# Optimization experiments

Measured on AMD Instinct MI355X. Metric: run time of the kernel, lower is better.

The kernel has to match this reference:

```python
import jax, jax.numpy as jnp
import numpy as np
from jax import lax

N_NODES, IN_FEATS = 10000, 768
B, P, MAXLEN = 2048, 16384, 50
V, D, NF, HID = 50000, 300, 100, 64


def setup_inputs() -> dict:
    key = jax.random.key(0)
    ks = jax.random.split(key, 17)
    emb = jax.random.normal(ks[4], (V, D), jnp.float32) * 0.1
    emb = emb.at[0].set(0.0)  # padding_idx=0
    return {
        'x': jax.random.normal(ks[0], (N_NODES, IN_FEATS), jnp.float32),
        'rootindex': jax.random.randint(ks[1], (B,), 0, N_NODES),
        'hist_tokens': jax.random.randint(ks[2], (P, MAXLEN), 0, V),
        'segment_ids': jnp.sort(jax.random.randint(ks[3], (P,), 0, B)),
        'emb_table': emb,
        'conv_w3': jax.random.normal(ks[5], (NF, D, 3), jnp.float32) * 0.02,
        'conv_b3': jax.random.normal(ks[6], (NF,), jnp.float32) * 0.02,
        'conv_w4': jax.random.normal(ks[7], (NF, D, 4), jnp.float32) * 0.02,
        'conv_b4': jax.random.normal(ks[8], (NF,), jnp.float32) * 0.02,
        'conv_w5': jax.random.normal(ks[9], (NF, D, 5), jnp.float32) * 0.02,
        'conv_b5': jax.random.normal(ks[10], (NF,), jnp.float32) * 0.02,
        'hist_w': jax.random.normal(ks[11], (HID, 3 * NF), jnp.float32) * 0.05,
        'hist_b': jax.random.normal(ks[12], (HID,), jnp.float32) * 0.02,
        'fc_w1': jax.random.normal(ks[13], (2 * HID, IN_FEATS), jnp.float32) * 0.03,
        'fc_b1': jax.random.normal(ks[14], (2 * HID,), jnp.float32) * 0.02,
        'fc_w2': jax.random.normal(ks[15], (HID, 2 * HID), jnp.float32) * 0.08,
        'fc_b2': jax.random.normal(ks[16], (HID,), jnp.float32) * 0.02,
    }


def reference(x, rootindex, hist_tokens, segment_ids, emb_table,
              conv_w3, conv_b3, conv_w4, conv_b4, conv_w5, conv_b5,
              hist_w, hist_b, fc_w1, fc_b1, fc_w2, fc_b2):
    nseg = rootindex.shape[0]  # B users
    # --- hist_aggregation: ragged per-user embedding lookup + mean over posts ---
    emb = emb_table[hist_tokens]                                   # [P, L, D]
    sums = jax.ops.segment_sum(emb, segment_ids, num_segments=nseg)  # [B, L, D]
    counts = jax.ops.segment_sum(jnp.ones((segment_ids.shape[0],), emb.dtype),
                                 segment_ids, num_segments=nseg)
    hist = sums / jnp.maximum(counts, 1.0)[:, None, None]          # [B, L, D]
    # --- records_aggregation: TextCNN over [B, D, L] ---
    xr = jnp.transpose(hist, (0, 2, 1))                            # [B, D, L]
    feats = []
    for w, b in ((conv_w3, conv_b3), (conv_w4, conv_b4), (conv_w5, conv_b5)):
        c = lax.conv_general_dilated(xr, w, (1,), 'VALID',
                                     dimension_numbers=('NCH', 'OIH', 'NCH'))
        c = jax.nn.relu(c + b[None, :, None])                      # [B, NF, L-K+1]
        feats.append(jnp.max(c, axis=-1))                          # global max pool
    f = jnp.concatenate(feats, axis=1)                             # [B, 3*NF]
    rec = f @ hist_w.T + hist_b                                    # [B, 64]
    # --- fc_out on root node features (dropout = eval no-op) ---
    h = jax.nn.relu(x[rootindex] @ fc_w1.T + fc_b1)                # [B, 128]
    out_fc = h @ fc_w2.T + fc_b2                                   # [B, 64]
    return rec + out_fc
```

## Files before the change

### kernel.cpp

```cpp
#include <hip/hip_runtime.h>

#define NB    2048
#define NP    16384
#define LL    50
#define DD    300
#define DP    320
#define TP    52
#define NTOT  300
#define NPADF 320
#define INFEAT 768
#define HID2  128
#define UPB   4
#define FCM   16

typedef short v8s __attribute__((ext_vector_type(8)));
typedef float v4f __attribute__((ext_vector_type(4)));
typedef float v2f __attribute__((ext_vector_type(2)));
typedef unsigned short v4u __attribute__((ext_vector_type(4)));

__device__ __forceinline__ unsigned short f2bf(float f) {
    union { float f; unsigned u; } v; v.f = f;
    return (unsigned short)((v.u + 0x7FFF + ((v.u >> 16) & 1)) >> 16);
}
__device__ __forceinline__ float bf2f(unsigned short u) {
    union { unsigned u; float f; } v; v.u = ((unsigned)u) << 16; return v.f;
}
__device__ __forceinline__ int lower_bound_i(const int* __restrict__ a, int n, int v) {
    int lo = 0, hi = n;
    while (lo < hi) { int mid = (lo + hi) >> 1; if (a[mid] < v) lo = mid + 1; else hi = mid; }
    return lo;
}

__device__ __forceinline__ void async_copy16(const void* g, void* l) {
    __builtin_amdgcn_global_load_lds(
        (const __attribute__((address_space(1))) unsigned int*)g,
        (__attribute__((address_space(3))) unsigned int*)l, 16, 0, 0);
}

__global__ void emb_cvt8(const float* __restrict__ in, unsigned* __restrict__ out, int n4) {
    for (int i = blockIdx.x * blockDim.x + threadIdx.x; i < n4; i += gridDim.x * blockDim.x) {
        float4 v = ((const float4*)in)[i];
        int o = 0;
        o = __builtin_amdgcn_cvt_pk_fp8_f32(v.x, v.y, o, false);
        o = __builtin_amdgcn_cvt_pk_fp8_f32(v.z, v.w, o, true);
        out[i] = (unsigned)o;
    }
}

__global__ void prep_w(const float* __restrict__ w3, const float* __restrict__ w4,
                       const float* __restrict__ w5,
                       const float* __restrict__ b3, const float* __restrict__ b4,
                       const float* __restrict__ b5,
                       unsigned short* __restrict__ W5f, float* __restrict__ bias_all,
                       const float* __restrict__ fw1, unsigned short* __restrict__ w1b) {
    int idx = blockIdx.x * blockDim.x + threadIdx.x;
    if (idx < HID2 * INFEAT / 4) {
        float4 v = ((const float4*)fw1)[idx];
        ushort4 o; o.x = f2bf(v.x); o.y = f2bf(v.y); o.z = f2bf(v.z); o.w = f2bf(v.w);
        ((ushort4*)w1b)[idx] = o;
    }
    if (idx < NPADF) {
        float bv = 0.f;
        if (idx < 100) bv = b3[idx];
        else if (idx < 200) bv = b4[idx - 100];
        else if (idx < 300) bv = b5[idx - 200];
        bias_all[idx] = bv;
    }
    if (idx >= 10 * 5 * 20 * 512) return;
    int j    = idx & 7;
    int lane = (idx >> 3) & 63;
    int rest = idx >> 9;
    int nt = rest % 20;
    int s  = (rest / 20) % 5;
    int kt = rest / 100;
    int col = lane & 15, quad = lane >> 4;
    int nf = nt * 16 + col;
    int d  = kt * 32 + quad * 8 + j;
    float v = 0.f;
    if (nf < NTOT && d < DD) {
        int cls = nf / 100, f = nf % 100, K = cls + 3;
        if (s < K) {
            const float* w = (cls == 0) ? w3 : (cls == 1) ? w4 : w5;
            v = w[(f * DD + d) * K + s];
        }
    }
    W5f[idx] = f2bf(v);
}

#define PCHUNK 32
__global__ __launch_bounds__(512, 1) void gather_kernel(
    const int* __restrict__ hist_tokens, const int* __restrict__ seg,
    const unsigned char* __restrict__ emb8, unsigned short* __restrict__ histb)
{
    __shared__ int tokoff[PCHUNK * LL];
    const int b = blockIdx.x, tid = threadIdx.x;
    const int lo = lower_bound_i(seg, NP, b);
    const int hi = lower_bound_i(seg, NP, b + 1);
    const float inv = 1.0f / fmaxf((float)(hi - lo), 1.0f);

    int toff[8], doff[8];
    #pragma unroll
    for (int j = 0; j < 8; ++j) {
        int idx = tid + 512 * j;
        if (idx < 3750) { toff[j] = idx / 75; doff[j] = (idx % 75) * 4; }
        else            { toff[j] = 0;        doff[j] = 0; }
    }
    const bool has8 = (tid < 166);

    float4 acc[8];
    #pragma unroll
    for (int j = 0; j < 8; ++j) acc[j] = make_float4(0.f, 0.f, 0.f, 0.f);

    for (int p0 = lo; p0 < hi; p0 += PCHUNK) {
        const int pc = min(PCHUNK, hi - p0);
        __syncthreads();
        for (int j = tid; j < pc * LL; j += 512)
            tokoff[j] = hist_tokens[p0 * LL + j] * DD;
        __syncthreads();
        int pp = 0;
        for (; pp + 1 < pc; pp += 2) {
            const int* trA = tokoff + pp * LL;
            const int* trB = trA + LL;
            unsigned va[8], vb[8];
            #pragma unroll
            for (int j = 0; j < 7; ++j)
                va[j] = *(const unsigned*)(emb8 + trA[toff[j]] + doff[j]);
            if (has8) va[7] = *(const unsigned*)(emb8 + trA[toff[7]] + doff[7]);
            #pragma unroll
            for (int j = 0; j < 7; ++j)
                vb[j] = *(const unsigned*)(emb8 + trB[toff[j]] + doff[j]);
            if (has8) vb[7] = *(const unsigned*)(emb8 + trB[toff[7]] + doff[7]);
            #pragma unroll
            for (int j = 0; j < 8; ++j) {
                if (j < 7 || has8) {
                    v2f la = __builtin_amdgcn_cvt_pk_f32_fp8(va[j], false);
                    v2f ha = __builtin_amdgcn_cvt_pk_f32_fp8(va[j], true);
                    v2f lb = __builtin_amdgcn_cvt_pk_f32_fp8(vb[j], false);
                    v2f hb2 = __builtin_amdgcn_cvt_pk_f32_fp8(vb[j], true);
                    acc[j].x += la[0] + lb[0];
                    acc[j].y += la[1] + lb[1];
                    acc[j].z += ha[0] + hb2[0];
                    acc[j].w += ha[1] + hb2[1];
                }
            }
        }
        if (pp < pc) {
            const int* tr = tokoff + pp * LL;
            unsigned v[8];
            #pragma unroll
            for (int j = 0; j < 7; ++j)
                v[j] = *(const unsigned*)(emb8 + tr[toff[j]] + doff[j]);
            if (has8) v[7] = *(const unsigned*)(emb8 + tr[toff[7]] + doff[7]);
            #pragma unroll
            for (int j = 0; j < 8; ++j) {
                if (j < 7 || has8) {
                    v2f lv = __builtin_amdgcn_cvt_pk_f32_fp8(v[j], false);
                    v2f hv = __builtin_amdgcn_cvt_pk_f32_fp8(v[j], true);
                    acc[j].x += lv[0]; acc[j].y += lv[1];
                    acc[j].z += hv[0]; acc[j].w += hv[1];
                }
            }
        }
    }

    unsigned short* hb = histb + (size_t)b * TP * DP;
    #pragma unroll
    for (int j = 0; j < 8; ++j) {
        if (j < 7 || has8) {
            v4u o;
            o[0] = f2bf(acc[j].x * inv); o[1] = f2bf(acc[j].y * inv);
            o[2] = f2bf(acc[j].z * inv); o[3] = f2bf(acc[j].w * inv);
            __builtin_nontemporal_store(o, (v4u*)(hb + toff[j] * DP + doff[j]));
        }
    }
    for (int i = tid; i < 640 + 1000; i += 512) {
        int t, d;
        if (i < 640) { t = 50 + i / 320; d = i % 320; }
        else         { int j = i - 640; t = j / 20; d = 300 + j % 20; }
        __builtin_nontemporal_store((unsigned short)0, hb + t * DP + d);
    }
}

__global__ __launch_bounds__(768, 3) void conv_kernel(
    const unsigned short* __restrict__ histb, const unsigned short* __restrict__ W5f,
    const float* __restrict__ bias_all,
    const float* __restrict__ hist_w, const float* __restrict__ hist_b,
    float* __restrict__ out)
{
    __shared__ __align__(16) unsigned short sA[UPB * 52 * 40];
    __shared__ __align__(16) unsigned short sBk[77 * 512];
    __shared__ __align__(16) float fpool[UPB * NPADF];

    const int b = blockIdx.x, tid = threadIdx.x;
    const int wave = tid >> 6, lane = tid & 63;
    const int col = lane & 15, quad = lane >> 4;
    const int u = wave & 3, g = wave >> 2;
    const int base = (g == 2) ? 14 : g * 7;
    const int cnt  = (g == 2) ? 5  : 7;

    const unsigned short* hbase = histb + (size_t)(b * UPB) * TP * DP;

    const int c0 = tid;
    const int a0_uu = c0 / 208, a0_r = c0 % 208;
    const int a0_row = a0_r >> 2, a0_ch = a0_r & 3;
    const int c1 = tid + 768;
    const int a1_uu = c1 / 208, a1_r = c1 % 208;
    const int a1_row = a1_r >> 2, a1_ch = a1_r & 3;
    const bool hasA1 = (tid < 64);

    v4f acc[3][7];
    #pragma unroll
    for (int m = 0; m < 3; ++m)
        #pragma unroll
        for (int j = 0; j < 7; ++j)
            acc[m][j] = (v4f){0.f, 0.f, 0.f, 0.f};

    v8s a0v, a1v;

    #define STAGE_B(KT)                                                              \
    {                                                                                \
        const unsigned short* wkt = W5f + (size_t)(KT) * 51200;                      \
        _Pragma("unroll")                                                            \
        for (int s5 = 0; s5 < 5; ++s5) {                                             \
            const int Ls  = (s5 < 3) ? 19 : (s5 == 3 ? 13 : 7);                      \
            const int los = (s5 < 3) ? 0  : (s5 == 3 ? 6  : 12);                     \
            const int cbs = (s5 < 3) ? 19 * s5 : (s5 == 3 ? 57 : 70);                \
            const unsigned short* srcs = wkt + s5 * 10240 + los * 512 + lane * 8;    \
            unsigned short* dsts = sBk + cbs * 512;                                  \
            if (wave < Ls)                                                           \
                async_copy16(srcs + wave * 512, dsts + wave * 512);                  \
            if (wave + 12 < Ls)                                                      \
                async_copy16(srcs + (wave + 12) * 512, dsts + (wave + 12) * 512);    \
        }                                                                            \
    }

    a0v = *(const v8s*)(hbase + (size_t)a0_uu * TP * DP + a0_row * DP + a0_ch * 8);
    if (hasA1)
        a1v = *(const v8s*)(hbase + (size_t)a1_uu * TP * DP + a1_row * DP + a1_ch * 8);
    STAGE_B(0);
    *(v8s*)(sA + (a0_uu * 52 + a0_row) * 40 + a0_ch * 8) = a0v;
    if (hasA1) *(v8s*)(sA + (a1_uu * 52 + a1_row) * 40 + a1_ch * 8) = a1v;
    __syncthreads();

    for (int kt = 0; kt < 10; ++kt) {
        if (kt < 9) {
            const int ko = (kt + 1) * 32;
            a0v = *(const v8s*)(hbase + (size_t)a0_uu * TP * DP + a0_row * DP + ko + a0_ch * 8);
            if (hasA1)
                a1v = *(const v8s*)(hbase + (size_t)a1_uu * TP * DP + a1_row * DP + ko + a1_ch * 8);
        }

        #pragma unroll
        for (int s = 0; s < 5; ++s) {
            const int lo  = (s == 3) ? 6 : (s == 4) ? 12 : 0;
            const int cbs = (s < 3) ? 19 * s : (s == 3 ? 57 : 70);

            const unsigned short* Arow = sA + (u * 52 + col + s) * 40 + quad * 8;
            const v8s am0 = *(const v8s*)(Arow);
            const v8s am1 = *(const v8s*)(Arow + 640);
            const v8s am2 = *(const v8s*)(Arow + 1280);
            #pragma unroll
            for (int j = 0; j < 7; ++j) {
                const int t = base + j;
                if (j < cnt && t >= lo) {
                    const int blk = cbs + (t - lo);
                    const v8s bf = *(const v8s*)(sBk + blk * 512 + lane * 8);
                    acc[0][j] = __builtin_amdgcn_mfma_f32_16x16x32_bf16(am0, bf, acc[0][j], 0, 0, 0);
                    acc[1][j] = __builtin_amdgcn_mfma_f32_16x16x32_bf16(am1, bf, acc[1][j], 0, 0, 0);
                    acc[2][j] = __builtin_amdgcn_mfma_f32_16x16x32_bf16(am2, bf, acc[2][j], 0, 0, 0);
                }
            }
        }

        if (kt < 9) {
            __syncthreads();
            STAGE_B(kt + 1);
            *(v8s*)(sA + (a0_uu * 52 + a0_row) * 40 + a0_ch * 8) = a0v;
            if (hasA1) *(v8s*)(sA + (a1_uu * 52 + a1_row) * 40 + a1_ch * 8) = a1v;
            __syncthreads();
        }
    }
    #undef STAGE_B

    #pragma unroll
    for (int j = 0; j < 7; ++j) {
        if (j < cnt) {
            const int nf = (base + j) * 16 + col;
            const int Tout = 48 - nf / 100;
            float mx = -1e30f;
            #pragma unroll
            for (int m = 0; m < 3; ++m)
                #pragma unroll
                for (int r = 0; r < 4; ++r) {
                    const int t = m * 16 + quad * 4 + r;
                    if (t < Tout) mx = fmaxf(mx, acc[m][j][r]);
                }
            mx = fmaxf(mx, __shfl_xor(mx, 16, 64));
            mx = fmaxf(mx, __shfl_xor(mx, 32, 64));
            if (quad == 0 && nf < NTOT)
                fpool[u * NPADF + nf] = fmaxf(0.f, mx + bias_all[nf]);
        }
    }
    __syncthreads();

    if (tid < UPB * 64) {
        const int uu = tid >> 6, o = tid & 63;
        const float4* fw = (const float4*)(hist_w + o * NTOT);
        const float4* fp = (const float4*)(fpool + uu * NPADF);
        float sum = 0.f;
        #pragma unroll
        for (int q = 0; q < NTOT / 4; ++q) {
            float4 aa = fp[q], ww = fw[q];
            sum += aa.x * ww.x + aa.y * ww.y + aa.z * ww.z + aa.w * ww.w;
        }
        out[(b * UPB + uu) * 64 + o] = sum + hist_b[o];
    }
}

__global__ __launch_bounds__(256, 1) void fc_mfma(
    const float* __restrict__ x, const int* __restrict__ rootindex,
    const unsigned short* __restrict__ w1b, const float* __restrict__ b1,
    const float* __restrict__ w2, const float* __restrict__ b2,
    float* __restrict__ out)
{
    __shared__ __align__(16) unsigned short sA[FCM * 72];
    __shared__ __align__(16) float hl[FCM * 132];
    __shared__ __align__(16) float w2l[64 * 129];
    __shared__ int roots[FCM];

    const int b = blockIdx.x, tid = threadIdx.x;
    if (tid < FCM) roots[tid] = rootindex[b * FCM + tid];
    for (int i = tid; i < 64 * HID2; i += 256)
        w2l[(i >> 7) * 129 + (i & 127)] = w2[i];
    __syncthreads();

    const int wave = tid >> 6, lane = tid & 63;
    const int col = lane & 15, quad = lane >> 4;

    v4f acc[2];
    acc[0] = (v4f){0.f, 0.f, 0.f, 0.f};
    acc[1] = (v4f){0.f, 0.f, 0.f, 0.f};

    const int r_st = tid >> 4, q_st = tid & 15;

    for (int kt = 0; kt < 12; ++kt) {
        __syncthreads();
        float4 v = *(const float4*)(x + (size_t)roots[r_st] * INFEAT + kt * 64 + q_st * 4);
        ushort4 o; o.x = f2bf(v.x); o.y = f2bf(v.y); o.z = f2bf(v.z); o.w = f2bf(v.w);
        *(ushort4*)(sA + r_st * 72 + q_st * 4) = o;
        __syncthreads();
        #pragma unroll
        for (int kc = 0; kc < 2; ++kc) {
            const v8s a = *(const v8s*)(sA + col * 72 + kc * 32 + quad * 8);
            #pragma unroll
            for (int n = 0; n < 2; ++n) {
                const int nf = (wave * 2 + n) * 16 + col;
                const v8s bfr = *(const v8s*)(w1b + (size_t)nf * INFEAT + kt * 64 + kc * 32 + quad * 8);
                acc[n] = __builtin_amdgcn_mfma_f32_16x16x32_bf16(a, bfr, acc[n], 0, 0, 0);
            }
        }
    }

    #pragma unroll
    for (int nt = 0; nt < 2; ++nt) {
        const int n = (wave * 2 + nt) * 16 + col;
        const float bv = b1[n];
        #pragma unroll
        for (int r = 0; r < 4; ++r)
            hl[(quad * 4 + r) * 132 + n] = fmaxf(acc[nt][r] + bv, 0.f);
    }
    __syncthreads();

    {
        const int o = tid & 63, ug = tid >> 6;
        const float b2v = b2[o];
        const float* wrow = w2l + o * 129;
        #pragma unroll
        for (int i = 0; i < 4; ++i) {
            const int u = ug * 4 + i;
            const float* hrow = hl + u * 132;
            float s = 0.f;
            #pragma unroll 16
            for (int k = 0; k < HID2; ++k) s += hrow[k] * wrow[k];
            out[(b * FCM + u) * 64 + o] += s + b2v;
        }
    }
}

extern "C" void kernel_launch(void* const* d_in, const int* in_sizes, int n_in,
                              void* d_out, int out_size, void* d_ws, size_t ws_size,
                              hipStream_t stream) {
    const float* x        = (const float*)d_in[0];
    const int*   rootidx  = (const int*)d_in[1];
    const int*   hist_tok = (const int*)d_in[2];
    const int*   seg      = (const int*)d_in[3];
    const float* emb      = (const float*)d_in[4];
    const float* w3       = (const float*)d_in[5];
    const float* cb3      = (const float*)d_in[6];
    const float* w4       = (const float*)d_in[7];
    const float* cb4      = (const float*)d_in[8];
    const float* w5       = (const float*)d_in[9];
    const float* cb5      = (const float*)d_in[10];
    const float* hist_w   = (const float*)d_in[11];
    const float* hist_b   = (const float*)d_in[12];
    const float* fw1      = (const float*)d_in[13];
    const float* fb1      = (const float*)d_in[14];
    const float* fw2      = (const float*)d_in[15];
    const float* fb2      = (const float*)d_in[16];
    float* out = (float*)d_out;

    char* ws = (char*)d_ws;
    unsigned char*  emb8    = (unsigned char*)(ws);
    unsigned short* hist_bf = (unsigned short*)(ws + 30000000);
    unsigned short* W5f     = (unsigned short*)(ws + 98157440);
    float*          bias_all= (float*)(ws + 99181440);
    unsigned short* w1b     = (unsigned short*)(ws + 99182720);

    emb_cvt8<<<2048, 256, 0, stream>>>(emb, (unsigned*)emb8, 50000 * DD / 4);
    prep_w<<<(10 * 5 * 20 * 512 + 255) / 256, 256, 0, stream>>>(
        w3, w4, w5, cb3, cb4, cb5, W5f, bias_all, fw1, w1b);
    gather_kernel<<<NB, 512, 0, stream>>>(hist_tok, seg, emb8, hist_bf);
    conv_kernel<<<NB / UPB, 768, 0, stream>>>(hist_bf, W5f, bias_all, hist_w, hist_b, out);
    fc_mfma<<<NB / FCM, 256, 0, stream>>>(x, rootidx, w1b, fb1, fw2, fb2, out);
}
```

Measured before the change: 302.3 us.

## Switch conv path to FP8 MFMA with packed weights and double-buffered LDS

The hist intermediate and the conv weights are now stored as FP8, scaled by 16 each, instead of bf16. The conv kernel uses 16x16x32 fp8 MFMA and rescales by 1/256 before the bias. Weights are prepacked into the compact per-kt block layout so the LDS copy becomes a plain contiguous copy. The A and B LDS tiles are double-buffered so staging the next tile overlaps compute, with one barrier per iteration instead of two. This halves the intermediate and weight traffic and LDS footprint, at the cost of extra quantization error on activations and weights.

```diff
diff --git a/kernel.cpp b/kernel.cpp
--- a/kernel.cpp
+++ b/kernel.cpp
@@ -4,7 +4,6 @@
 #define NP    16384
 #define LL    50
 #define DD    300
-#define DP    320
 #define TP    52
 #define NTOT  300
 #define NPADF 320
@@ -12,18 +11,15 @@
 #define HID2  128
 #define UPB   4
 #define FCM   16
+#define BKT   39936
 
 typedef short v8s __attribute__((ext_vector_type(8)));
 typedef float v4f __attribute__((ext_vector_type(4)));
 typedef float v2f __attribute__((ext_vector_type(2)));
-typedef unsigned short v4u __attribute__((ext_vector_type(4)));
 
 __device__ __forceinline__ unsigned short f2bf(float f) {
     union { float f; unsigned u; } v; v.f = f;
     return (unsigned short)((v.u + 0x7FFF + ((v.u >> 16) & 1)) >> 16);
-}
-__device__ __forceinline__ float bf2f(unsigned short u) {
-    union { unsigned u; float f; } v; v.u = ((unsigned)u) << 16; return v.f;
 }
 __device__ __forceinline__ int lower_bound_i(const int* __restrict__ a, int n, int v) {
     int lo = 0, hi = n;
@@ -47,13 +43,13 @@
     }
 }
 
-__global__ void prep_w(const float* __restrict__ w3, const float* __restrict__ w4,
-                       const float* __restrict__ w5,
-                       const float* __restrict__ b3, const float* __restrict__ b4,
-                       const float* __restrict__ b5,
-                       unsigned short* __restrict__ W5f, float* __restrict__ bias_all,
-                       const float* __restrict__ fw1, unsigned short* __restrict__ w1b) {
-    int idx = blockIdx.x * blockDim.x + threadIdx.x;
+__global__ void prep_w8(const float* __restrict__ w3, const float* __restrict__ w4,
+                        const float* __restrict__ w5,
+                        const float* __restrict__ b3, const float* __restrict__ b4,
+                        const float* __restrict__ b5,
+                        unsigned char* __restrict__ W5f8, float* __restrict__ bias_all,
+                        const float* __restrict__ fw1, unsigned short* __restrict__ w1b) {
+    const int idx = blockIdx.x * blockDim.x + threadIdx.x;
     if (idx < HID2 * INFEAT / 4) {
         float4 v = ((const float4*)fw1)[idx];
         ushort4 o; o.x = f2bf(v.x); o.y = f2bf(v.y); o.z = f2bf(v.z); o.w = f2bf(v.w);
@@ -66,37 +62,45 @@
         else if (idx < 300) bv = b5[idx - 200];
         bias_all[idx] = bv;
     }
-    if (idx >= 10 * 5 * 20 * 512) return;
-    int j    = idx & 7;
-    int lane = (idx >> 3) & 63;
-    int rest = idx >> 9;
-    int nt = rest % 20;
-    int s  = (rest / 20) % 5;
-    int kt = rest / 100;
-    int col = lane & 15, quad = lane >> 4;
-    int nf = nt * 16 + col;
-    int d  = kt * 32 + quad * 8 + j;
-    float v = 0.f;
-    if (nf < NTOT && d < DD) {
-        int cls = nf / 100, f = nf % 100, K = cls + 3;
+    if (idx < 10 * 128)
+        *(unsigned*)(W5f8 + (size_t)(idx >> 7) * BKT + 39424 + (idx & 127) * 4) = 0u;
+    if (idx >= 256000) return;
+    const int j2   = idx & 3;
+    const int lane = (idx >> 2) & 63;
+    const int rest = idx >> 8;
+    const int nt = rest % 20;
+    const int s  = (rest / 20) % 5;
+    const int kt = rest / 100;
+    const int lo = (s == 3) ? 6 : (s == 4) ? 12 : 0;
+    if (nt < lo || nt >= 19) return;
+    const int cbs = (s < 3) ? 19 * s : (s == 3 ? 57 : 70);
+    const int col = lane & 15, quad = lane >> 4;
+    const int nf = nt * 16 + col;
+    float v0 = 0.f, v1 = 0.f;
+    if (nf < NTOT) {
+        const int cls = nf / 100, f = nf % 100, K = cls + 3;
         if (s < K) {
             const float* w = (cls == 0) ? w3 : (cls == 1) ? w4 : w5;
-            v = w[(f * DD + d) * K + s];
-        }
-    }
-    W5f[idx] = f2bf(v);
+            const int d0 = kt * 32 + quad * 8 + j2 * 2;
+            if (d0 < DD)     v0 = 16.f * w[(f * DD + d0) * K + s];
+            if (d0 + 1 < DD) v1 = 16.f * w[(f * DD + d0 + 1) * K + s];
+        }
+    }
+    const int p = __builtin_amdgcn_cvt_pk_fp8_f32(v0, v1, 0, false);
+    *(unsigned short*)(W5f8 + (size_t)kt * BKT + (cbs + nt - lo) * 512 + lane * 8 + j2 * 2)
+        = (unsigned short)(p & 0xffff);
 }
 
 #define PCHUNK 32
 __global__ __launch_bounds__(512, 1) void gather_kernel(
     const int* __restrict__ hist_tokens, const int* __restrict__ seg,
-    const unsigned char* __restrict__ emb8, unsigned short* __restrict__ histb)
+    const unsigned char* __restrict__ emb8, unsigned char* __restrict__ hist8)
 {
     __shared__ int tokoff[PCHUNK * LL];
     const int b = blockIdx.x, tid = threadIdx.x;
     const int lo = lower_bound_i(seg, NP, b);
     const int hi = lower_bound_i(seg, NP, b + 1);
-    const float inv = 1.0f / fmaxf((float)(hi - lo), 1.0f);
+    const float inv16 = 16.f / fmaxf((float)(hi - lo), 1.0f);
 
     int toff[8], doff[8];
     #pragma unroll
@@ -163,32 +167,32 @@
         }
     }
 
-    unsigned short* hb = histb + (size_t)b * TP * DP;
+    unsigned char* hb = hist8 + (size_t)b * TP * 320;
     #pragma unroll
     for (int j = 0; j < 8; ++j) {
         if (j < 7 || has8) {
-            v4u o;
-            o[0] = f2bf(acc[j].x * inv); o[1] = f2bf(acc[j].y * inv);
-            o[2] = f2bf(acc[j].z * inv); o[3] = f2bf(acc[j].w * inv);
-            __builtin_nontemporal_store(o, (v4u*)(hb + toff[j] * DP + doff[j]));
-        }
-    }
-    for (int i = tid; i < 640 + 1000; i += 512) {
-        int t, d;
-        if (i < 640) { t = 50 + i / 320; d = i % 320; }
-        else         { int j = i - 640; t = j / 20; d = 300 + j % 20; }
-        __builtin_nontemporal_store((unsigned short)0, hb + t * DP + d);
+            int p = 0;
+            p = __builtin_amdgcn_cvt_pk_fp8_f32(acc[j].x * inv16, acc[j].y * inv16, p, false);
+            p = __builtin_amdgcn_cvt_pk_fp8_f32(acc[j].z * inv16, acc[j].w * inv16, p, true);
+            __builtin_nontemporal_store((unsigned)p, (unsigned*)(hb + toff[j] * 320 + doff[j]));
+        }
+    }
+    for (int i = tid; i < 410; i += 512) {
+        unsigned char* p;
+        if (i < 160) { const int t = 50 + i / 80; p = hb + t * 320 + (i % 80) * 4; }
+        else         { const int j = i - 160; p = hb + (j / 5) * 320 + 300 + (j % 5) * 4; }
+        __builtin_nontemporal_store(0u, (unsigned*)p);
     }
 }
 
 __global__ __launch_bounds__(768, 3) void conv_kernel(
-    const unsigned short* __restrict__ histb, const unsigned short* __restrict__ W5f,
+    const unsigned char* __restrict__ histb, const unsigned char* __restrict__ W5f8,
     const float* __restrict__ bias_all,
     const float* __restrict__ hist_w, const float* __restrict__ hist_b,
     float* __restrict__ out)
 {
-    __shared__ __align__(16) unsigned short sA[UPB * 52 * 40];
-    __shared__ __align__(16) unsigned short sBk[77 * 512];
+    __shared__ __align__(16) unsigned char sA[2][208 * 40];
+    __shared__ __align__(16) unsigned char sB[2][BKT];
     __shared__ __align__(16) float fpool[UPB * NPADF];
 
     const int b = blockIdx.x, tid = threadIdx.x;
@@ -198,14 +202,10 @@
     const int base = (g == 2) ? 14 : g * 7;
     const int cnt  = (g == 2) ? 5  : 7;
 
-    const unsigned short* hbase = histb + (size_t)(b * UPB) * TP * DP;
-
-    const int c0 = tid;
-    const int a0_uu = c0 / 208, a0_r = c0 % 208;
-    const int a0_row = a0_r >> 2, a0_ch = a0_r & 3;
-    const int c1 = tid + 768;
-    const int a1_uu = c1 / 208, a1_r = c1 % 208;
-    const int a1_row = a1_r >> 2, a1_ch = a1_r & 3;
+    const unsigned char* hbase = histb + (size_t)(b * UPB) * TP * 320;
+
+    const int r0 = tid >> 2, ch0 = tid & 3;
+    const int r1 = (tid + 768) >> 2;
     const bool hasA1 = (tid < 64);
 
     v4f acc[3][7];
@@ -215,72 +215,64 @@
         for (int j = 0; j < 7; ++j)
             acc[m][j] = (v4f){0.f, 0.f, 0.f, 0.f};
 
-    v8s a0v, a1v;
-
-    #define STAGE_B(KT)                                                              \
-    {                                                                                \
-        const unsigned short* wkt = W5f + (size_t)(KT) * 51200;                      \
-        _Pragma("unroll")                                                            \
-        for (int s5 = 0; s5 < 5; ++s5) {                                             \
-            const int Ls  = (s5 < 3) ? 19 : (s5 == 3 ? 13 : 7);                      \
-            const int los = (s5 < 3) ? 0  : (s5 == 3 ? 6  : 12);                     \
-            const int cbs = (s5 < 3) ? 19 * s5 : (s5 == 3 ? 57 : 70);                \
-            const unsigned short* srcs = wkt + s5 * 10240 + los * 512 + lane * 8;    \
-            unsigned short* dsts = sBk + cbs * 512;                                  \
-            if (wave < Ls)                                                           \
-                async_copy16(srcs + wave * 512, dsts + wave * 512);                  \
-            if (wave + 12 < Ls)                                                      \
-                async_copy16(srcs + (wave + 12) * 512, dsts + (wave + 12) * 512);    \
-        }                                                                            \
-    }
-
-    a0v = *(const v8s*)(hbase + (size_t)a0_uu * TP * DP + a0_row * DP + a0_ch * 8);
-    if (hasA1)
-        a1v = *(const v8s*)(hbase + (size_t)a1_uu * TP * DP + a1_row * DP + a1_ch * 8);
-    STAGE_B(0);
-    *(v8s*)(sA + (a0_uu * 52 + a0_row) * 40 + a0_ch * 8) = a0v;
-    if (hasA1) *(v8s*)(sA + (a1_uu * 52 + a1_row) * 40 + a1_ch * 8) = a1v;
+    unsigned long long a0v, a1v = 0;
+
+    #define STAGE_B8(KT, BUF)                                                      \
+    {                                                                              \
+        const unsigned char* _src = W5f8 + (size_t)(KT) * BKT + lane * 16;         \
+        unsigned char* _dst = sB[BUF];                                             \
+        async_copy16(_src + wave * 1024,        _dst + wave * 1024);               \
+        async_copy16(_src + (wave + 12) * 1024, _dst + (wave + 12) * 1024);        \
+        async_copy16(_src + (wave + 24) * 1024, _dst + (wave + 24) * 1024);        \
+        if (wave < 3)                                                              \
+            async_copy16(_src + (wave + 36) * 1024, _dst + (wave + 36) * 1024);    \
+    }
+
+    a0v = *(const unsigned long long*)(hbase + r0 * 320 + ch0 * 8);
+    if (hasA1) a1v = *(const unsigned long long*)(hbase + r1 * 320 + ch0 * 8);
+    STAGE_B8(0, 0);
+    *(unsigned long long*)(sA[0] + r0 * 40 + ch0 * 8) = a0v;
+    if (hasA1) *(unsigned long long*)(sA[0] + r1 * 40 + ch0 * 8) = a1v;
     __syncthreads();
+    a0v = *(const unsigned long long*)(hbase + r0 * 320 + 32 + ch0 * 8);
+    if (hasA1) a1v = *(const unsigned long long*)(hbase + r1 * 320 + 32 + ch0 * 8);
 
     for (int kt = 0; kt < 10; ++kt) {
+        const int cur = kt & 1;
         if (kt < 9) {
-            const int ko = (kt + 1) * 32;
-            a0v = *(const v8s*)(hbase + (size_t)a0_uu * TP * DP + a0_row * DP + ko + a0_ch * 8);
-            if (hasA1)
-                a1v = *(const v8s*)(hbase + (size_t)a1_uu * TP * DP + a1_row * DP + ko + a1_ch * 8);
-        }
+            STAGE_B8(kt + 1, cur ^ 1);
+            *(unsigned long long*)(sA[cur ^ 1] + r0 * 40 + ch0 * 8) = a0v;
+            if (hasA1) *(unsigned long long*)(sA[cur ^ 1] + r1 * 40 + ch0 * 8) = a1v;
+            if (kt < 8) {
+                const int ko = (kt + 2) * 32;
+                a0v = *(const unsigned long long*)(hbase + r0 * 320 + ko + ch0 * 8);
+                if (hasA1) a1v = *(const unsigned long long*)(hbase + r1 * 320 + ko + ch0 * 8);
+            }
+        }
+        __builtin_amdgcn_sched_barrier(0);
 
         #pragma unroll
         for (int s = 0; s < 5; ++s) {
             const int lo  = (s == 3) ? 6 : (s == 4) ? 12 : 0;
             const int cbs = (s < 3) ? 19 * s : (s == 3 ? 57 : 70);
-
-            const unsigned short* Arow = sA + (u * 52 + col + s) * 40 + quad * 8;
-            const v8s am0 = *(const v8s*)(Arow);
-            const v8s am1 = *(const v8s*)(Arow + 640);
-            const v8s am2 = *(const v8s*)(Arow + 1280);
+            const unsigned char* Ab = sA[cur] + (u * 52 + col + s) * 40 + quad * 8;
+            const long am0 = *(const long*)(Ab);
+            const long am1 = *(const long*)(Ab + 640);
+            const long am2 = *(const long*)(Ab + 1280);
             #pragma unroll
             for (int j = 0; j < 7; ++j) {
                 const int t = base + j;
                 if (j < cnt && t >= lo) {
-                    const int blk = cbs + (t - lo);
-                    const v8s bf = *(const v8s*)(sBk + blk * 512 + lane * 8);
-                    acc[0][j] = __builtin_amdgcn_mfma_f32_16x16x32_bf16(am0, bf, acc[0][j], 0, 0, 0);
-                    acc[1][j] = __builtin_amdgcn_mfma_f32_16x16x32_bf16(am1, bf, acc[1][j], 0, 0, 0);
-                    acc[2][j] = __builtin_amdgcn_mfma_f32_16x16x32_bf16(am2, bf, acc[2][j], 0, 0, 0);
+                    const long bf = *(const long*)(sB[cur] + (cbs + t - lo) * 512 + lane * 8);
+                    acc[0][j] = __builtin_amdgcn_mfma_f32_16x16x32_fp8_fp8(am0, bf, acc[0][j], 0, 0, 0);
+                    acc[1][j] = __builtin_amdgcn_mfma_f32_16x16x32_fp8_fp8(am1, bf, acc[1][j], 0, 0, 0);
+                    acc[2][j] = __builtin_amdgcn_mfma_f32_16x16x32_fp8_fp8(am2, bf, acc[2][j], 0, 0, 0);
                 }
             }
         }
-
-        if (kt < 9) {
-            __syncthreads();
-            STAGE_B(kt + 1);
-            *(v8s*)(sA + (a0_uu * 52 + a0_row) * 40 + a0_ch * 8) = a0v;
-            if (hasA1) *(v8s*)(sA + (a1_uu * 52 + a1_row) * 40 + a1_ch * 8) = a1v;
-            __syncthreads();
-        }
-    }
-    #undef STAGE_B
+        if (kt < 9) __syncthreads();
+    }
+    #undef STAGE_B8
 
     #pragma unroll
     for (int j = 0; j < 7; ++j) {
@@ -298,7 +290,7 @@
             mx = fmaxf(mx, __shfl_xor(mx, 16, 64));
             mx = fmaxf(mx, __shfl_xor(mx, 32, 64));
             if (quad == 0 && nf < NTOT)
-                fpool[u * NPADF + nf] = fmaxf(0.f, mx + bias_all[nf]);
+                fpool[u * NPADF + nf] = fmaxf(0.f, mx * (1.f / 256.f) + bias_all[nf]);
         }
     }
     __syncthreads();
@@ -411,15 +403,15 @@
 
     char* ws = (char*)d_ws;
     unsigned char*  emb8    = (unsigned char*)(ws);
-    unsigned short* hist_bf = (unsigned short*)(ws + 30000000);
-    unsigned short* W5f     = (unsigned short*)(ws + 98157440);
+    unsigned char*  hist8   = (unsigned char*)(ws + 30000000);
+    unsigned char*  W5f8    = (unsigned char*)(ws + 98157440);
     float*          bias_all= (float*)(ws + 99181440);
     unsigned short* w1b     = (unsigned short*)(ws + 99182720);
 
     emb_cvt8<<<2048, 256, 0, stream>>>(emb, (unsigned*)emb8, 50000 * DD / 4);
-    prep_w<<<(10 * 5 * 20 * 512 + 255) / 256, 256, 0, stream>>>(
-        w3, w4, w5, cb3, cb4, cb5, W5f, bias_all, fw1, w1b);
-    gather_kernel<<<NB, 512, 0, stream>>>(hist_tok, seg, emb8, hist_bf);
-    conv_kernel<<<NB / UPB, 768, 0, stream>>>(hist_bf, W5f, bias_all, hist_w, hist_b, out);
+    prep_w8<<<1000, 256, 0, stream>>>(
+        w3, w4, w5, cb3, cb4, cb5, W5f8, bias_all, fw1, w1b);
+    gather_kernel<<<NB, 512, 0, stream>>>(hist_tok, seg, emb8, hist8);
+    conv_kernel<<<NB / UPB, 768, 0, stream>>>(hist8, W5f8, bias_all, hist_w, hist_b, out);
     fc_mfma<<<NB / FCM, 256, 0, stream>>>(x, rootidx, w1b, fb1, fw2, fb2, out);
 }
```

Result: faster. 282.8 us (-6.5%).
